# Performance work log

Hardware: AMD Instinct MI355X
Metric: run time of the kernel (lower is better)

Reference implementation:

```python
import jax, jax.numpy as jnp
import numpy as np

EPS = 2e-05
N_H_RDG = 9   # lifting scale grid: h_j = 2**j, j=0..8
N_H_CROP = 3  # group-conv scale support: offsets 0,1,2 (dyadic index shifts)


def _scaled_kernel(w, h):
    """Resample base kernel w [O, I, K] (taps on integers centered at 0) at
    coordinates x/h via linear interpolation -> [O, I, (K-1)*h+1], with the
    R+ Haar-measure normalization 1/h (psi_h(x) = psi(x/h)/h)."""
    K = w.shape[-1]
    Kh = (K - 1) * h + 1
    m = jnp.arange(K, dtype=jnp.float32) - K // 2
    x = (jnp.arange(Kh, dtype=jnp.float32) - Kh // 2) / h
    hat = jnp.maximum(0.0, 1.0 - jnp.abs(x[:, None] - m[None, :]))  # [Kh, K]
    return jnp.einsum('oim,xm->oix', w, hat) / h


def _conv1d_same(x, k):
    pad = (k.shape[-1] - 1) // 2
    return jax.lax.conv_general_dilated(
        x, k, window_strides=(1,), padding=[(pad, pad)],
        dimension_numbers=('NCH', 'OIH', 'NCH'))


def _pool_r1(x, stride):
    # max pool over the spatial (last) axis only: kernel 4, pad 1 each side
    return jax.lax.reduce_window(
        x, -jnp.inf, jax.lax.max,
        window_dimensions=(1, 1, 1, 4), window_strides=(1, 1, 1, stride),
        padding=((0, 0), (0, 0), (0, 0), (1, 1)))


def _bn(x, g, b):
    # BatchNorm2d over [B, C, H_scale, L], training-mode batch stats
    mu = jnp.mean(x, axis=(0, 2, 3), keepdims=True)
    var = jnp.var(x, axis=(0, 2, 3), keepdims=True)
    return (x - mu) * jax.lax.rsqrt(var + EPS) * g[None, :, None, None] + b[None, :, None, None]


def _forward(x, w1, w2, w3, g1, b1, g2, b2, g3, b3, fw1, fb1, fw2, fb2, fw3, fb3):
    B = x.shape[0]
    # --- c1: GConvRdG lifting, scales h_j = 2**j, j=0..8 ---
    out = jnp.stack([_conv1d_same(x, _scaled_kernel(w1, 2 ** j))
                     for j in range(N_H_RDG)], axis=2)      # [B,16,9,16]
    out = _bn(jax.nn.relu(_pool_r1(out, 2)), g1, b1)        # [B,16,9,8]
    # --- c2: GConvGG, h_crop=True: out scale j uses in scales j..j+2 ---
    O2, I2 = w2.shape[0], w2.shape[1]
    w2r = w2.reshape(O2, I2 * N_H_CROP, 3)
    H2 = out.shape[2] - (N_H_CROP - 1)  # 7
    out = jnp.stack([
        _conv1d_same(out[:, :, j:j + N_H_CROP, :].reshape(B, I2 * N_H_CROP, -1),
                     _scaled_kernel(w2r, 2 ** j))
        for j in range(H2)], axis=2)                        # [B,32,7,8]
    out = _bn(jax.nn.relu(_pool_r1(out, 2)), g2, b2)        # [B,32,7,4]
    # --- c3: GConvGG with 1x1 spatial kernel ---
    w3s = w3[:, :, :, 0]  # [64,32,3]
    H3 = out.shape[2] - (N_H_CROP - 1)  # 5
    out = jnp.stack([
        jnp.einsum('oik,bikl->bol', w3s, out[:, :, j:j + N_H_CROP, :]) / (2.0 ** j)
        for j in range(H3)], axis=2)                        # [B,64,5,4]
    out = _bn(jax.nn.relu(_pool_r1(out, 4)), g3, b3)        # [B,64,5,1]
    # --- MLP head (dropout is identity in eval) ---
    out = out.reshape(B, -1)                                # [B,320]
    out = out @ fw1.T + fb1
    out = out @ fw2.T + fb2
    return out @ fw3.T + fb3                                # [B,17]


def setup_inputs() -> dict:
    key = jax.random.key(0)
    ks = jax.random.split(key, 7)
    B = 4096
    x = jax.random.normal(ks[0], (B, 6, 16), dtype=jnp.float32)
    w1 = jax.random.normal(ks[1], (16, 6, 7), dtype=jnp.float32) * (6 * 7) ** -0.5
    w2 = jax.random.normal(ks[2], (32, 16, 3, 3), dtype=jnp.float32) * (16 * 3 * 3) ** -0.5
    w3 = jax.random.normal(ks[3], (64, 32, 3, 1), dtype=jnp.float32) * (32 * 3) ** -0.5
    fw1 = jax.random.normal(ks[4], (16, 320), dtype=jnp.float32) * 320 ** -0.5
    fw2 = jax.random.normal(ks[5], (16, 16), dtype=jnp.float32) * 16 ** -0.5
    fw3 = jax.random.normal(ks[6], (17, 16), dtype=jnp.float32) * 16 ** -0.5
    return {
        'x': x, 'w1': w1, 'w2': w2, 'w3': w3,
        'g1': jnp.ones(16), 'b1': jnp.zeros(16),
        'g2': jnp.ones(32), 'b2': jnp.zeros(32),
        'g3': jnp.ones(64), 'b3': jnp.zeros(64),
        'fw1': fw1, 'fb1': jnp.zeros(16),
        'fw2': fw2, 'fb2': jnp.zeros(16),
        'fw3': fw3, 'fb3': jnp.zeros(17),
    }


def reference(x, w1, w2, w3, g1, b1, g2, b2, g3, b3, fw1, fb1, fw2, fb2, fw3, fb3):
    return _forward(x, w1, w2, w3, g1, b1, g2, b2, g3, b3, fw1, fb1, fw2, fb2, fw3, fb3)
```

## Files before the change

kernel.cpp:

```cpp
#include <hip/hip_runtime.h>

#define EPS 2e-5f

using short8  = __attribute__((ext_vector_type(8))) short;
using floatx4 = __attribute__((ext_vector_type(4))) float;

static __device__ inline unsigned short f2bf(float f) {
    unsigned u = __float_as_uint(f);
    u += 0x7fffu + ((u >> 16) & 1u);
    return (unsigned short)(u >> 16);
}


__global__ void __launch_bounds__(256) k_setup(const float* __restrict__ w1,
                                               unsigned short* __restrict__ W1f,
                                               float* __restrict__ stats) {
    int gid = blockIdx.x * 256 + threadIdx.x;
    if (gid < 256) stats[gid] = 0.f;
    if (gid >= 221184) return;
    int j  = gid / 24576;
    int r  = gid % 24576;
    int T  = r / 1536;
    int r2 = r % 1536;
    int ks = r2 / 512;
    int r3 = r2 % 512;
    int lane = r3 >> 3, e = r3 & 7;
    int n  = T * 16 + (lane & 15);
    int kk = ks * 32 + (lane >> 4) * 8 + e;
    int o = n >> 4, t = n & 15;
    int i = kk >> 4, s = kk & 15;
    int h = 1 << j;
    int d = s - t;
    float val = 0.f;
    if (d >= -3 * h && d <= 3 * h) {
        float df = (float)d / (float)h;
        #pragma unroll
        for (int m = 0; m < 7; ++m) {
            float hat = fmaxf(0.f, 1.f - fabsf(df - (float)(m - 3)));
            val += w1[(o * 6 + i) * 7 + m] * hat;
        }
        val /= (float)h;
    }
    W1f[gid] = f2bf(val);
}

__global__ void __launch_bounds__(256) k1(const float* __restrict__ x,
                                          const unsigned short* __restrict__ W1f,
                                          unsigned short* __restrict__ p1,
                                          float* __restrict__ stats1) {
    int j    = blockIdx.y;
    int wav  = threadIdx.x >> 6;
    int lane = threadIdx.x & 63;
    int msub = wav & 1, nh = wav >> 1;
    int mt   = blockIdx.x * 2 + msub;
    int quad = lane >> 4, l15 = lane & 15;
    floatx4 z = {0.f, 0.f, 0.f, 0.f};
    floatx4 acc[8];
    #pragma unroll
    for (int T = 0; T < 8; ++T) acc[T] = z;
    const float* xr = x + (size_t)(mt * 16 + l15) * 96;
    const short8* Bj = (const short8*)W1f + (size_t)(j * 16) * 3 * 64;
    #pragma unroll
    for (int ks = 0; ks < 3; ++ks) {
        int k0 = ks * 32 + quad * 8;
        floatx4 v0 = *(const floatx4*)(xr + k0);
        floatx4 v1 = *(const floatx4*)(xr + k0 + 4);
        short8 a;
        #pragma unroll
        for (int e = 0; e < 4; ++e) {
            a[e]     = (short)f2bf(v0[e]);
            a[e + 4] = (short)f2bf(v1[e]);
        }
        #pragma unroll
        for (int T = 0; T < 8; ++T) {
            short8 b = Bj[((nh * 8 + T) * 3 + ks) * 64 + lane];
            acc[T] = __builtin_amdgcn_mfma_f32_16x16x32_bf16(a, b, acc[T], 0, 0, 0);
        }
    }
    __shared__ float ls[32];
    if (threadIdx.x < 32) ls[threadIdx.x] = 0.f;
    __syncthreads();
    int mbase = mt * 16 + quad * 4;
    int tp = l15;
    bool act = tp < 8;
    int tpe = tp & 7;
    int base = lane & 48;
    int c0 = base + max(2 * tpe - 1, 0);
    int c1 = base + 2 * tpe;
    int c2 = base + 2 * tpe + 1;
    int c3 = base + min(2 * tpe + 2, 15);
    #pragma unroll
    for (int T = 0; T < 8; ++T) {
        int o = nh * 8 + T;
        float psum = 0.f, pss = 0.f;
        #pragma unroll
        for (int r = 0; r < 4; ++r) {
            float v  = acc[T][r];
            float mx = fmaxf(fmaxf(__shfl(v, c0, 64), __shfl(v, c1, 64)),
                             fmaxf(__shfl(v, c2, 64), __shfl(v, c3, 64)));
            mx = fmaxf(mx, 0.f);
            if (act) {
                p1[(size_t)(mbase + r) * 1152 + o * 72 + j * 8 + tp] = f2bf(mx);
                psum += mx; pss += mx * mx;
            }
        }
        #pragma unroll
        for (int m = 32; m >= 1; m >>= 1) {
            psum += __shfl_xor(psum, m, 64);
            pss  += __shfl_xor(pss,  m, 64);
        }
        if (lane == 0) {
            atomicAdd(&ls[o], psum);
            atomicAdd(&ls[16 + o], pss);
        }
    }
    __syncthreads();
    if (threadIdx.x < 16) {
        atomicAdd(&stats1[threadIdx.x], ls[threadIdx.x]);
        atomicAdd(&stats1[16 + threadIdx.x], ls[16 + threadIdx.x]);
    }
}

__global__ void __launch_bounds__(384) k_bias(const float* __restrict__ w2,
                                              const float* __restrict__ g1,
                                              const float* __restrict__ b1,
                                              const float* __restrict__ stats1,
                                              unsigned short* __restrict__ W2f,
                                              float* __restrict__ bias2,
                                              float invN1) {
    int blk = blockIdx.x;
    int j   = blk >> 8;
    int col = blk & 255;
    int o = col >> 3, t = col & 7;
    int k = threadIdx.x;
    int ic = k >> 3, s = k & 7;
    int i = ic / 3, c = ic % 3;
    float mu  = stats1[i] * invN1;
    float var = stats1[16 + i] * invN1 - mu * mu;
    float rsg = rsqrtf(var + EPS);
    float a1  = g1[i] * rsg;
    float d1  = b1[i] - mu * a1;
    int h = 1 << j;
    int d = s - t;
    float raw = 0.f;
    if (d >= -h && d <= h) {
        float df = (float)d / (float)h;
        #pragma unroll
        for (int m = 0; m < 3; ++m) {
            float hat = fmaxf(0.f, 1.f - fabsf(df - (float)(m - 1)));
            raw += w2[((o * 16 + i) * 3 + c) * 3 + m] * hat;
        }
        raw /= (float)h;
    }
    {
        int T    = col >> 4;
        int lane = (col & 15) + ((k >> 3) & 3) * 16;
        int ks   = k >> 5;
        int e    = k & 7;
        W2f[(((size_t)(j * 16 + T) * 12 + ks) * 64 + lane) * 8 + e] = f2bf(raw * a1);
    }
    __shared__ float red[384];
    red[k] = raw * d1;
    __syncthreads();
    if (k < 128) red[k] += red[k + 128] + red[k + 256];
    __syncthreads();
    for (int st = 64; st >= 1; st >>= 1) {
        if (k < st) red[k] += red[k + st];
        __syncthreads();
    }
    if (k == 0) bias2[j * 256 + col] = red[0];
}

__global__ void __launch_bounds__(256) k2(const unsigned short* __restrict__ p1,
                                          const unsigned short* __restrict__ W2f,
                                          const float* __restrict__ bias2,
                                          unsigned short* __restrict__ p2s,
                                          float* __restrict__ stats2,
                                          int B) {
    int j    = blockIdx.y;
    int wav  = threadIdx.x >> 6;
    int lane = threadIdx.x & 63;
    int nh   = wav & 1, mp = wav >> 1;
    int m0   = blockIdx.x * 64 + mp * 32;
    int quad = lane >> 4, l15 = lane & 15;
    floatx4 z = {0.f, 0.f, 0.f, 0.f};
    floatx4 acc[2][8];
    #pragma unroll
    for (int mi = 0; mi < 2; ++mi)
        #pragma unroll
        for (int T = 0; T < 8; ++T) acc[mi][T] = z;
    const short8* Bj = (const short8*)W2f + (size_t)(j * 16) * 12 * 64;
    const unsigned short* Arow0 = p1 + (size_t)(m0 + l15) * 1152;
    const unsigned short* Arow1 = Arow0 + 16 * 1152;
    #pragma unroll
    for (int ks = 0; ks < 12; ++ks) {
        int k0 = ks * 32 + quad * 8;
        int i  = k0 / 24;
        int c  = (k0 - i * 24) >> 3;
        int off = i * 72 + (j + c) * 8;
        short8 a0 = *(const short8*)(Arow0 + off);
        short8 a1 = *(const short8*)(Arow1 + off);
        #pragma unroll
        for (int T = 0; T < 8; ++T) {
            short8 b = Bj[((nh * 8 + T) * 12 + ks) * 64 + lane];
            acc[0][T] = __builtin_amdgcn_mfma_f32_16x16x32_bf16(a0, b, acc[0][T], 0, 0, 0);
            acc[1][T] = __builtin_amdgcn_mfma_f32_16x16x32_bf16(a1, b, acc[1][T], 0, 0, 0);
        }
    }
    __shared__ float ls[64];
    if (threadIdx.x < 64) ls[threadIdx.x] = 0.f;
    __syncthreads();
    int tp  = lane & 7;
    bool act = tp < 4;
    int tpe = tp & 3;
    int base = lane & 56;
    int c0 = base + max(2 * tpe - 1, 0);
    int c1 = base + 2 * tpe;
    int c2 = base + 2 * tpe + 1;
    int c3 = base + min(2 * tpe + 2, 7);
    #pragma unroll
    for (int T = 0; T < 8; ++T) {
        int n = (nh * 8 + T) * 16 + l15;
        int o = n >> 3;
        float bias = bias2[j * 256 + n];
        float psum = 0.f, pss = 0.f;
        #pragma unroll
        for (int mi = 0; mi < 2; ++mi) {
            int mbase = m0 + mi * 16 + quad * 4;
            #pragma unroll
            for (int r = 0; r < 4; ++r) {
                float v  = acc[mi][T][r] + bias;
                float mx = fmaxf(fmaxf(__shfl(v, c0, 64), __shfl(v, c1, 64)),
                                 fmaxf(__shfl(v, c2, 64), __shfl(v, c3, 64)));
                mx = fmaxf(mx, 0.f);
                if (act) {
                    p2s[(((size_t)j * 4 + tp) * B + mbase + r) * 32 + o] = f2bf(mx);
                    psum += mx; pss += mx * mx;
                }
            }
        }
        #pragma unroll
        for (int m = 0; m < 5; ++m) {
            int msk = (m < 3) ? (1 << m) : (1 << (m + 1));
            psum += __shfl_xor(psum, msk, 64);
            pss  += __shfl_xor(pss,  msk, 64);
        }
        if (lane == 0 || lane == 8) {
            int oo = (nh * 8 + T) * 2 + (lane >> 3);
            atomicAdd(&ls[oo], psum);
            atomicAdd(&ls[32 + oo], pss);
        }
    }
    __syncthreads();
    if (threadIdx.x < 32) {
        atomicAdd(&stats2[threadIdx.x], ls[threadIdx.x]);
        atomicAdd(&stats2[32 + threadIdx.x], ls[32 + threadIdx.x]);
    }
}

__global__ void __launch_bounds__(256) k3(const unsigned short* __restrict__ p2s,
                                          const float* __restrict__ w3,
                                          const float* __restrict__ g2,
                                          const float* __restrict__ b2,
                                          const float* __restrict__ stats2,
                                          float* __restrict__ act3,
                                          float* __restrict__ stats3,
                                          float invN2, int B) {
    int j    = blockIdx.y;
    int wav  = threadIdx.x >> 6;
    int lane = threadIdx.x & 63;
    int msub = wav & 1, nh = wav >> 1;
    int m0   = (blockIdx.x * 2 + msub) * 16;
    int quad = lane >> 4, l15 = lane & 15;
    __shared__ float a2s[32], d2s[32], bias3s[64], ls[128];
    __shared__ unsigned short W3s[6144];
    if (threadIdx.x < 128) ls[threadIdx.x] = 0.f;
    if (threadIdx.x < 32) {
        int i = threadIdx.x;
        float mu  = stats2[i] * invN2;
        float var = stats2[32 + i] * invN2 - mu * mu;
        float rsg = rsqrtf(var + EPS);
        a2s[i] = g2[i] * rsg;
        d2s[i] = b2[i] - mu * a2s[i];
    }
    __syncthreads();
    for (int idx = threadIdx.x; idx < 6144; idx += 256) {
        int e  = idx & 7;
        int ln = (idx >> 3) & 63;
        int fs = idx >> 9;
        int Tg = fs / 3, ks = fs % 3;
        int n = Tg * 16 + (ln & 15);
        int i = (ln >> 4) * 8 + e;
        W3s[idx] = f2bf(w3[n * 96 + i * 3 + ks] * a2s[i]);
    }
    if (threadIdx.x < 64) {
        float s = 0.f;
        for (int i = 0; i < 32; ++i)
            #pragma unroll
            for (int kk = 0; kk < 3; ++kk)
                s = fmaf(w3[threadIdx.x * 96 + i * 3 + kk], d2s[i], s);
        bias3s[threadIdx.x] = s;
    }
    __syncthreads();
    short8 bf[2][3];
    #pragma unroll
    for (int T = 0; T < 2; ++T)
        #pragma unroll
        for (int ks = 0; ks < 3; ++ks)
            bf[T][ks] = *(const short8*)&W3s[(((nh * 2 + T) * 3 + ks) * 64 + lane) * 8];
    floatx4 z = {0.f, 0.f, 0.f, 0.f};
    floatx4 acc[2][3];
    #pragma unroll
    for (int T = 0; T < 2; ++T)
        #pragma unroll
        for (int l = 0; l < 3; ++l) acc[T][l] = z;
    #pragma unroll
    for (int ks = 0; ks < 3; ++ks) {
        int jj = j + ks;
        #pragma unroll
        for (int l = 0; l < 3; ++l) {
            const short8* ap =
                (const short8*)(p2s + ((size_t)(jj * 4 + l) * B + m0 + l15) * 32) + quad;
            short8 a = *ap;
            #pragma unroll
            for (int T = 0; T < 2; ++T)
                acc[T][l] = __builtin_amdgcn_mfma_f32_16x16x32_bf16(a, bf[T][ks],
                                                                    acc[T][l], 0, 0, 0);
        }
    }
    float inv = 1.f / (float)(1 << j);
    int mbase = m0 + quad * 4;
    #pragma unroll
    for (int T = 0; T < 2; ++T) {
        int col = nh * 32 + T * 16 + l15;
        float bias = bias3s[col];
        float psum = 0.f, pss = 0.f;
        #pragma unroll
        for (int r = 0; r < 4; ++r) {
            float v = fmaxf(fmaxf(acc[T][0][r], acc[T][1][r]), acc[T][2][r]);
            v = fmaxf((v + bias) * inv, 0.f);
            act3[(size_t)(mbase + r) * 320 + col * 5 + j] = v;
            psum += v; pss += v * v;
        }
        psum += __shfl_xor(psum, 16, 64); pss += __shfl_xor(pss, 16, 64);
        psum += __shfl_xor(psum, 32, 64); pss += __shfl_xor(pss, 32, 64);
        if (quad == 0) {
            atomicAdd(&ls[col], psum);
            atomicAdd(&ls[64 + col], pss);
        }
    }
    __syncthreads();
    if (threadIdx.x < 64) {
        atomicAdd(&stats3[threadIdx.x], ls[threadIdx.x]);
        atomicAdd(&stats3[64 + threadIdx.x], ls[64 + threadIdx.x]);
    }
}

__global__ void __launch_bounds__(128) k4(const float* __restrict__ act3,
                                          const float* __restrict__ g3,
                                          const float* __restrict__ b3,
                                          const float* __restrict__ stats3,
                                          const float* __restrict__ fw1,
                                          const float* __restrict__ fb1,
                                          const float* __restrict__ fw2,
                                          const float* __restrict__ fb2,
                                          const float* __restrict__ fw3,
                                          const float* __restrict__ fb3,
                                          float* __restrict__ out,
                                          float invN3) {
    __shared__ float a3s[64], d3s[64];
    __shared__ unsigned short W1s[5120];
    __shared__ float fw2s[256], fw3s[272], fb2s[16], fb3s[17], fb1f[16];
    __shared__ float hbuf[2][16][17];
    int tid = threadIdx.x;
    if (tid < 64) {
        float mu  = stats3[tid] * invN3;
        float var = stats3[64 + tid] * invN3 - mu * mu;
        float rsg = rsqrtf(var + EPS);
        a3s[tid] = g3[tid] * rsg;
        d3s[tid] = b3[tid] - mu * a3s[tid];
    }
    __syncthreads();
    for (int idx = tid; idx < 5120; idx += 128) {
        int e  = idx & 7;
        int ln = (idx >> 3) & 63;
        int ks = idx >> 9;
        int n  = ln & 15;
        int k  = ks * 32 + (ln >> 4) * 8 + e;
        W1s[idx] = f2bf(fw1[n * 320 + k] * a3s[k / 5]);
    }
    for (int idx = tid; idx < 256; idx += 128) fw2s[idx] = fw2[idx];
    for (int idx = tid; idx < 272; idx += 128) fw3s[idx] = fw3[idx];
    if (tid < 16) fb2s[tid] = fb2[tid];
    if (tid < 17) fb3s[tid] = fb3[tid];
    if (tid < 16) {
        float s = fb1[tid];
        for (int o = 0; o < 64; ++o) {
            float dd = d3s[o];
            #pragma unroll
            for (int jj = 0; jj < 5; ++jj)
                s = fmaf(fw1[tid * 320 + o * 5 + jj], dd, s);
        }
        fb1f[tid] = s;
    }
    __syncthreads();
    int wav = tid >> 6, lane = tid & 63;
    int quad = lane >> 4, l15 = lane & 15;
    int mt = blockIdx.x * 2 + wav;
    const float* ar = act3 + (size_t)(mt * 16 + l15) * 320;
    floatx4 acc = {0.f, 0.f, 0.f, 0.f};
    #pragma unroll
    for (int ks = 0; ks < 10; ++ks) {
        int k0 = ks * 32 + quad * 8;
        floatx4 v0 = *(const floatx4*)(ar + k0);
        floatx4 v1 = *(const floatx4*)(ar + k0 + 4);
        short8 a;
        #pragma unroll
        for (int e = 0; e < 4; ++e) {
            a[e]     = (short)f2bf(v0[e]);
            a[e + 4] = (short)f2bf(v1[e]);
        }
        short8 b = *(const short8*)&W1s[(ks * 64 + lane) * 8];
        acc = __builtin_amdgcn_mfma_f32_16x16x32_bf16(a, b, acc, 0, 0, 0);
    }
    #pragma unroll
    for (int r = 0; r < 4; ++r)
        hbuf[wav][quad * 4 + r][l15] = acc[r] + fb1f[l15];
    __syncthreads();
    if (lane < 16) {
        int row = l15;
        float hv[16];
        #pragma unroll
        for (int n = 0; n < 16; ++n) hv[n] = hbuf[wav][row][n];
        float h2[16];
        #pragma unroll
        for (int f2 = 0; f2 < 16; ++f2) {
            float s = fb2s[f2];
            #pragma unroll
            for (int n = 0; n < 16; ++n) s = fmaf(fw2s[f2 * 16 + n], hv[n], s);
            h2[f2] = s;
        }
        float* orow = out + (size_t)(mt * 16 + row) * 17;
        #pragma unroll
        for (int f3 = 0; f3 < 17; ++f3) {
            float s = fb3s[f3];
            #pragma unroll
            for (int n = 0; n < 16; ++n) s = fmaf(fw3s[f3 * 16 + n], h2[n], s);
            orow[f3] = s;
        }
    }
}

extern "C" void kernel_launch(void* const* d_in, const int* in_sizes, int n_in,
                              void* d_out, int out_size, void* d_ws, size_t ws_size,
                              hipStream_t stream) {
    (void)n_in; (void)out_size; (void)ws_size;
    const float* x   = (const float*)d_in[0];
    const float* w1  = (const float*)d_in[1];
    const float* w2  = (const float*)d_in[2];
    const float* w3  = (const float*)d_in[3];
    const float* g1  = (const float*)d_in[4];
    const float* b1  = (const float*)d_in[5];
    const float* g2  = (const float*)d_in[6];
    const float* b2  = (const float*)d_in[7];
    const float* g3  = (const float*)d_in[8];
    const float* b3  = (const float*)d_in[9];
    const float* fw1 = (const float*)d_in[10];
    const float* fb1 = (const float*)d_in[11];
    const float* fw2 = (const float*)d_in[12];
    const float* fb2 = (const float*)d_in[13];
    const float* fw3 = (const float*)d_in[14];
    const float* fb3 = (const float*)d_in[15];
    float* out = (float*)d_out;

    int B = in_sizes[0] / 96;

    char* wsb = (char*)d_ws;
    float*          stats  = (float*)wsb;
    unsigned short* W1f    = (unsigned short*)(wsb + 1024);
    unsigned short* W2f    = W1f + 221184;
    float*          bias2  = (float*)(W2f + 688128);
    unsigned short* p1     = (unsigned short*)(bias2 + 1792);
    unsigned short* p2s    = p1 + (size_t)B * 1152;
    float*          act3   = (float*)(p2s + (size_t)B * 896);

    float* stats1 = stats;
    float* stats2 = stats + 32;
    float* stats3 = stats + 96;

    float invN1 = 1.f / (float)(B * 72);
    float invN2 = 1.f / (float)(B * 28);
    float invN3 = 1.f / (float)(B * 5);

    k_setup<<<864, 256, 0, stream>>>(w1, W1f, stats);
    k1<<<dim3(B / 32, 9), 256, 0, stream>>>(x, W1f, p1, stats1);
    k_bias<<<7 * 256, 384, 0, stream>>>(w2, g1, b1, stats1, W2f, bias2, invN1);
    k2<<<dim3(B / 64, 7), 256, 0, stream>>>(p1, W2f, bias2, p2s, stats2, B);
    k3<<<dim3(B / 32, 5), 256, 0, stream>>>(p2s, w3, g2, b2, stats2, act3, stats3,
                                            invN2, B);
    k4<<<B / 32, 128, 0, stream>>>(act3, g3, b3, stats3, fw1, fb1, fw2, fb2, fw3, fb3,
                                   out, invN3);
}
```

Baseline: 204.1 us.

## Fuse all stages into one cooperative persistent kernel with grid syncs

Replaces the six separate kernel launches with a single cooperative persistent kernel that runs every stage in turn and separates them with grid-wide syncs. It also changes the intermediate layouts to scale-major bf16 tiles, written coalesced through shared memory, and stores act3 as bf16 instead of fp32. The aim is to remove launch gaps and shrink intermediate memory traffic. In exchange it pays for grid barriers and limits parallelism to the number of resident blocks, capped at 512.

```diff
diff --git a/kernel.cpp b/kernel.cpp
--- a/kernel.cpp
+++ b/kernel.cpp
@@ -1,6 +1,9 @@
 #include <hip/hip_runtime.h>
+#include <hip/hip_cooperative_groups.h>
 
 #define EPS 2e-5f
+
+namespace cg = cooperative_groups;
 
 using short8  = __attribute__((ext_vector_type(8))) short;
 using floatx4 = __attribute__((ext_vector_type(4))) float;
@@ -12,441 +15,485 @@
 }
 
 
-__global__ void __launch_bounds__(256) k_setup(const float* __restrict__ w1,
-                                               unsigned short* __restrict__ W1f,
-                                               float* __restrict__ stats) {
-    int gid = blockIdx.x * 256 + threadIdx.x;
-    if (gid < 256) stats[gid] = 0.f;
-    if (gid >= 221184) return;
-    int j  = gid / 24576;
-    int r  = gid % 24576;
-    int T  = r / 1536;
-    int r2 = r % 1536;
-    int ks = r2 / 512;
-    int r3 = r2 % 512;
-    int lane = r3 >> 3, e = r3 & 7;
-    int n  = T * 16 + (lane & 15);
-    int kk = ks * 32 + (lane >> 4) * 8 + e;
-    int o = n >> 4, t = n & 15;
-    int i = kk >> 4, s = kk & 15;
-    int h = 1 << j;
-    int d = s - t;
-    float val = 0.f;
-    if (d >= -3 * h && d <= 3 * h) {
-        float df = (float)d / (float)h;
+struct P2S { float ls[32]; unsigned short ptile[32][16][8]; };
+struct P3S { float a1[16]; float d1[16]; };
+struct P4S { float ls[64]; unsigned short ptile[4][64][32]; };
+struct P5S { float a2s[32], d2s[32], bias3s[64], ls[128];
+             unsigned short W3s[6144]; unsigned short atile[32][64]; };
+struct P6S { float a3s[64], d3s[64];
+             float fw2s[256], fw3s[272], fb2s[16], fb3s[17], fb1f[16];
+             float hbuf[4][16][17]; unsigned short W1s[5120]; };
+union SmemU { P2S p2; P3S p3; P4S p4; P5S p5; P6S p6; };
+
+__global__ void __launch_bounds__(256, 2)
+mega(const float* __restrict__ x,   const float* __restrict__ w1,
+     const float* __restrict__ w2,  const float* __restrict__ w3,
+     const float* __restrict__ g1,  const float* __restrict__ b1,
+     const float* __restrict__ g2,  const float* __restrict__ b2,
+     const float* __restrict__ g3,  const float* __restrict__ b3,
+     const float* __restrict__ fw1, const float* __restrict__ fb1,
+     const float* __restrict__ fw2, const float* __restrict__ fb2,
+     const float* __restrict__ fw3, const float* __restrict__ fb3,
+     float* __restrict__ out,
+     float* __restrict__ stats, unsigned short* __restrict__ W1f,
+     unsigned short* __restrict__ W2f, float* __restrict__ bias2,
+     unsigned short* __restrict__ p1, unsigned short* __restrict__ p2s,
+     unsigned short* __restrict__ act3, int B) {
+    cg::grid_group gg = cg::this_grid();
+    __shared__ SmemU sm;
+    const int tid  = threadIdx.x;
+    const int bid  = blockIdx.x;
+    const int nblk = gridDim.x;
+    const int wav  = tid >> 6;
+    const int lane = tid & 63;
+    const int quad = lane >> 4, l15 = lane & 15;
+    float* stats1 = stats;
+    float* stats2 = stats + 32;
+    float* stats3 = stats + 96;
+    const float invN1 = 1.f / (float)(B * 72);
+    const float invN2 = 1.f / (float)(B * 28);
+    const float invN3 = 1.f / (float)(B * 5);
+
+    {
+        int g0 = bid * 256 + tid;
+        if (g0 < 256) stats[g0] = 0.f;
+        for (int gid = g0; gid < 221184; gid += nblk * 256) {
+            int j  = gid / 24576;
+            int r  = gid % 24576;
+            int T  = r / 1536;
+            int r2 = r % 1536;
+            int ks = r2 / 512;
+            int r3 = r2 % 512;
+            int ln = r3 >> 3, e = r3 & 7;
+            int n  = T * 16 + (ln & 15);
+            int kk = ks * 32 + (ln >> 4) * 8 + e;
+            int o = n >> 4, t = n & 15;
+            int i = kk >> 4, s = kk & 15;
+            int h = 1 << j;
+            int d = s - t;
+            float val = 0.f;
+            if (d >= -3 * h && d <= 3 * h) {
+                float df = (float)d / (float)h;
+                #pragma unroll
+                for (int m = 0; m < 7; ++m) {
+                    float hat = fmaxf(0.f, 1.f - fabsf(df - (float)(m - 3)));
+                    val += w1[(o * 6 + i) * 7 + m] * hat;
+                }
+                val /= (float)h;
+            }
+            W1f[gid] = f2bf(val);
+        }
+    }
+    gg.sync();
+
+    {
+        int t32max = B / 32;
+        int msub = wav & 1, nh = wav >> 1;
+        for (int wi = bid; wi < 9 * t32max; wi += nblk) {
+            int j = wi / t32max, t32 = wi - j * t32max;
+            __syncthreads();
+            if (tid < 32) sm.p2.ls[tid] = 0.f;
+            int mt = t32 * 2 + msub;
+            floatx4 z = {0.f, 0.f, 0.f, 0.f};
+            floatx4 acc[8];
+            #pragma unroll
+            for (int T = 0; T < 8; ++T) acc[T] = z;
+            const float* xr = x + (size_t)(mt * 16 + l15) * 96;
+            const short8* Bj = (const short8*)W1f + (size_t)(j * 16) * 3 * 64;
+            #pragma unroll
+            for (int ks = 0; ks < 3; ++ks) {
+                int k0 = ks * 32 + quad * 8;
+                floatx4 v0 = *(const floatx4*)(xr + k0);
+                floatx4 v1 = *(const floatx4*)(xr + k0 + 4);
+                short8 a;
+                #pragma unroll
+                for (int e = 0; e < 4; ++e) {
+                    a[e]     = (short)f2bf(v0[e]);
+                    a[e + 4] = (short)f2bf(v1[e]);
+                }
+                #pragma unroll
+                for (int T = 0; T < 8; ++T) {
+                    short8 b = Bj[((nh * 8 + T) * 3 + ks) * 64 + lane];
+                    acc[T] = __builtin_amdgcn_mfma_f32_16x16x32_bf16(a, b, acc[T], 0, 0, 0);
+                }
+            }
+            __syncthreads();
+            int tp = l15;
+            bool act = tp < 8;
+            int tpe = tp & 7;
+            int base = lane & 48;
+            int c0 = base + max(2 * tpe - 1, 0);
+            int c1 = base + 2 * tpe;
+            int c2 = base + 2 * tpe + 1;
+            int c3 = base + min(2 * tpe + 2, 15);
+            int row_l = msub * 16 + quad * 4;
+            #pragma unroll
+            for (int T = 0; T < 8; ++T) {
+                int o = nh * 8 + T;
+                float psum = 0.f, pss = 0.f;
+                #pragma unroll
+                for (int r = 0; r < 4; ++r) {
+                    float v  = acc[T][r];
+                    float mx = fmaxf(fmaxf(__shfl(v, c0, 64), __shfl(v, c1, 64)),
+                                     fmaxf(__shfl(v, c2, 64), __shfl(v, c3, 64)));
+                    mx = fmaxf(mx, 0.f);
+                    if (act) {
+                        sm.p2.ptile[row_l + r][o][tp] = f2bf(mx);
+                        psum += mx; pss += mx * mx;
+                    }
+                }
+                #pragma unroll
+                for (int m = 32; m >= 1; m >>= 1) {
+                    psum += __shfl_xor(psum, m, 64);
+                    pss  += __shfl_xor(pss,  m, 64);
+                }
+                if (lane == 0) {
+                    atomicAdd(&sm.p2.ls[o], psum);
+                    atomicAdd(&sm.p2.ls[16 + o], pss);
+                }
+            }
+            __syncthreads();
+            unsigned short* dst = p1 + ((size_t)j * B + t32 * 32) * 128;
+            #pragma unroll
+            for (int u = 0; u < 2; ++u) {
+                int c = tid + u * 256;
+                int rr = c >> 4, oo = c & 15;
+                *(short8*)(dst + (size_t)rr * 128 + oo * 8) =
+                    *(const short8*)&sm.p2.ptile[rr][oo][0];
+            }
+            if (tid < 16) {
+                atomicAdd(&stats1[tid], sm.p2.ls[tid]);
+                atomicAdd(&stats1[16 + tid], sm.p2.ls[16 + tid]);
+            }
+        }
+    }
+    gg.sync();
+
+    {
+        if (tid < 16) {
+            float mu  = stats1[tid] * invN1;
+            float var = stats1[16 + tid] * invN1 - mu * mu;
+            float rsg = rsqrtf(var + EPS);
+            float a1  = g1[tid] * rsg;
+            sm.p3.a1[tid] = a1;
+            sm.p3.d1[tid] = b1[tid] - mu * a1;
+        }
+        __syncthreads();
+        for (int gid = bid * 256 + tid; gid < 688128; gid += nblk * 256) {
+            int j  = gid / 98304;
+            int r  = gid % 98304;
+            int T  = r / 6144;
+            int r2 = r % 6144;
+            int ks = r2 / 512;
+            int r3 = r2 % 512;
+            int ln = r3 >> 3, e = r3 & 7;
+            int col = T * 16 + (ln & 15);
+            int k   = ks * 32 + ((ln >> 4) << 3) + e;
+            int o = col >> 3, t = col & 7;
+            int ic = k >> 3, s = k & 7;
+            int i = ic / 3, c = ic % 3;
+            int h = 1 << j;
+            int d = s - t;
+            float raw = 0.f;
+            if (d >= -h && d <= h) {
+                float df = (float)d / (float)h;
+                #pragma unroll
+                for (int m = 0; m < 3; ++m) {
+                    float hat = fmaxf(0.f, 1.f - fabsf(df - (float)(m - 1)));
+                    raw += w2[((o * 16 + i) * 3 + c) * 3 + m] * hat;
+                }
+                raw /= (float)h;
+            }
+            W2f[gid] = f2bf(raw * sm.p3.a1[i]);
+        }
+        for (int e = bid * 4 + wav; e < 1792; e += nblk * 4) {
+            int j = e >> 8, col = e & 255;
+            int o = col >> 3, t = col & 7;
+            int h = 1 << j;
+            float s = 0.f;
+            #pragma unroll
+            for (int u = 0; u < 6; ++u) {
+                int k = lane + 64 * u;
+                int ic = k >> 3, ss = k & 7;
+                int i = ic / 3, c = ic % 3;
+                int d = ss - t;
+                float raw = 0.f;
+                if (d >= -h && d <= h) {
+                    float df = (float)d / (float)h;
+                    #pragma unroll
+                    for (int m = 0; m < 3; ++m) {
+                        float hat = fmaxf(0.f, 1.f - fabsf(df - (float)(m - 1)));
+                        raw += w2[((o * 16 + i) * 3 + c) * 3 + m] * hat;
+                    }
+                    raw /= (float)h;
+                }
+                s = fmaf(raw, sm.p3.d1[i], s);
+            }
+            #pragma unroll
+            for (int m = 32; m >= 1; m >>= 1) s += __shfl_xor(s, m, 64);
+            if (lane == 0) bias2[e] = s;
+        }
+    }
+    gg.sync();
+
+    {
+        int t64max = B / 64;
+        int nh = wav & 1, mp = wav >> 1;
+        for (int wi = bid; wi < 7 * t64max; wi += nblk) {
+            int j = wi / t64max, t64 = wi - j * t64max;
+            __syncthreads();
+            if (tid < 64) sm.p4.ls[tid] = 0.f;
+            int m0 = t64 * 64 + mp * 32;
+            floatx4 z = {0.f, 0.f, 0.f, 0.f};
+            floatx4 acc[2][8];
+            #pragma unroll
+            for (int mi = 0; mi < 2; ++mi)
+                #pragma unroll
+                for (int T = 0; T < 8; ++T) acc[mi][T] = z;
+            const short8* Bj = (const short8*)W2f + (size_t)(j * 16) * 12 * 64;
+            #pragma unroll
+            for (int ks = 0; ks < 12; ++ks) {
+                int k0 = ks * 32 + quad * 8;
+                int i  = k0 / 24;
+                int c  = (k0 - i * 24) >> 3;
+                const unsigned short* ab =
+                    p1 + ((size_t)(j + c) * B + m0 + l15) * 128 + i * 8;
+                short8 a0 = *(const short8*)ab;
+                short8 a1 = *(const short8*)(ab + 16 * 128);
+                #pragma unroll
+                for (int T = 0; T < 8; ++T) {
+                    short8 b = Bj[((nh * 8 + T) * 12 + ks) * 64 + lane];
+                    acc[0][T] = __builtin_amdgcn_mfma_f32_16x16x32_bf16(a0, b, acc[0][T], 0, 0, 0);
+                    acc[1][T] = __builtin_amdgcn_mfma_f32_16x16x32_bf16(a1, b, acc[1][T], 0, 0, 0);
+                }
+            }
+            __syncthreads();
+            int tp  = lane & 7;
+            bool act = tp < 4;
+            int tpe = tp & 3;
+            int base = lane & 56;
+            int c0 = base + max(2 * tpe - 1, 0);
+            int c1 = base + 2 * tpe;
+            int c2 = base + 2 * tpe + 1;
+            int c3 = base + min(2 * tpe + 2, 7);
+            #pragma unroll
+            for (int T = 0; T < 8; ++T) {
+                int n = (nh * 8 + T) * 16 + l15;
+                int o = n >> 3;
+                float bias = bias2[j * 256 + n];
+                float psum = 0.f, pss = 0.f;
+                #pragma unroll
+                for (int mi = 0; mi < 2; ++mi) {
+                    int rbase = mp * 32 + mi * 16 + quad * 4;
+                    #pragma unroll
+                    for (int r = 0; r < 4; ++r) {
+                        float v  = acc[mi][T][r] + bias;
+                        float mx = fmaxf(fmaxf(__shfl(v, c0, 64), __shfl(v, c1, 64)),
+                                         fmaxf(__shfl(v, c2, 64), __shfl(v, c3, 64)));
+                        mx = fmaxf(mx, 0.f);
+                        if (act) {
+                            sm.p4.ptile[tp][rbase + r][o] = f2bf(mx);
+                            psum += mx; pss += mx * mx;
+                        }
+                    }
+                }
+                #pragma unroll
+                for (int m = 0; m < 5; ++m) {
+                    int msk = (m < 3) ? (1 << m) : (1 << (m + 1));
+                    psum += __shfl_xor(psum, msk, 64);
+                    pss  += __shfl_xor(pss,  msk, 64);
+                }
+                if (lane == 0 || lane == 8) {
+                    int oo = (nh * 8 + T) * 2 + (lane >> 3);
+                    atomicAdd(&sm.p4.ls[oo], psum);
+                    atomicAdd(&sm.p4.ls[32 + oo], pss);
+                }
+            }
+            __syncthreads();
+            #pragma unroll
+            for (int u = 0; u < 4; ++u) {
+                int c = tid + u * 256;
+                int tpp = c >> 8, rem = c & 255;
+                int rr = rem >> 2, oq = rem & 3;
+                *(short8*)(p2s + ((size_t)(j * 4 + tpp) * B + t64 * 64 + rr) * 32 + oq * 8) =
+                    *(const short8*)&sm.p4.ptile[tpp][rr][oq * 8];
+            }
+            if (tid < 32) {
+                atomicAdd(&stats2[tid], sm.p4.ls[tid]);
+                atomicAdd(&stats2[32 + tid], sm.p4.ls[32 + tid]);
+            }
+        }
+    }
+    gg.sync();
+
+    {
+        if (tid < 32) {
+            float mu  = stats2[tid] * invN2;
+            float var = stats2[32 + tid] * invN2 - mu * mu;
+            float rsg = rsqrtf(var + EPS);
+            sm.p5.a2s[tid] = g2[tid] * rsg;
+            sm.p5.d2s[tid] = b2[tid] - mu * sm.p5.a2s[tid];
+        }
+        __syncthreads();
+        for (int idx = tid; idx < 6144; idx += 256) {
+            int e  = idx & 7;
+            int ln = (idx >> 3) & 63;
+            int fs = idx >> 9;
+            int Tg = fs / 3, ks = fs % 3;
+            int n = Tg * 16 + (ln & 15);
+            int i = (ln >> 4) * 8 + e;
+            sm.p5.W3s[idx] = f2bf(w3[n * 96 + i * 3 + ks] * sm.p5.a2s[i]);
+        }
+        if (tid < 64) {
+            float s = 0.f;
+            for (int i = 0; i < 32; ++i)
+                #pragma unroll
+                for (int kk = 0; kk < 3; ++kk)
+                    s = fmaf(w3[tid * 96 + i * 3 + kk], sm.p5.d2s[i], s);
+            sm.p5.bias3s[tid] = s;
+        }
+        __syncthreads();
+        int msub = wav & 1, nh = wav >> 1;
+        short8 bf[2][3];
         #pragma unroll
-        for (int m = 0; m < 7; ++m) {
-            float hat = fmaxf(0.f, 1.f - fabsf(df - (float)(m - 3)));
-            val += w1[(o * 6 + i) * 7 + m] * hat;
-        }
-        val /= (float)h;
+        for (int T = 0; T < 2; ++T)
+            #pragma unroll
+            for (int ks = 0; ks < 3; ++ks)
+                bf[T][ks] = *(const short8*)&sm.p5.W3s[(((nh * 2 + T) * 3 + ks) * 64 + lane) * 8];
+        int t32max = B / 32;
+        for (int wi = bid; wi < 5 * t32max; wi += nblk) {
+            int j = wi / t32max, t32 = wi - j * t32max;
+            __syncthreads();
+            if (tid < 128) sm.p5.ls[tid] = 0.f;
+            int m0 = (t32 * 2 + msub) * 16;
+            floatx4 z = {0.f, 0.f, 0.f, 0.f};
+            floatx4 acc[2][3];
+            #pragma unroll
+            for (int T = 0; T < 2; ++T)
+                #pragma unroll
+                for (int l = 0; l < 3; ++l) acc[T][l] = z;
+            #pragma unroll
+            for (int ks = 0; ks < 3; ++ks) {
+                int jj = j + ks;
+                #pragma unroll
+                for (int l = 0; l < 3; ++l) {
+                    short8 a = *(const short8*)(p2s +
+                        ((size_t)(jj * 4 + l) * B + m0 + l15) * 32 + quad * 8);
+                    #pragma unroll
+                    for (int T = 0; T < 2; ++T)
+                        acc[T][l] = __builtin_amdgcn_mfma_f32_16x16x32_bf16(a, bf[T][ks],
+                                                                            acc[T][l], 0, 0, 0);
+                }
+            }
+            __syncthreads();
+            float inv = 1.f / (float)(1 << j);
+            int row_l = msub * 16 + quad * 4;
+            #pragma unroll
+            for (int T = 0; T < 2; ++T) {
+                int col = nh * 32 + T * 16 + l15;
+                float bias = sm.p5.bias3s[col];
+                float psum = 0.f, pss = 0.f;
+                #pragma unroll
+                for (int r = 0; r < 4; ++r) {
+                    float v = fmaxf(fmaxf(acc[T][0][r], acc[T][1][r]), acc[T][2][r]);
+                    v = fmaxf((v + bias) * inv, 0.f);
+                    sm.p5.atile[row_l + r][col] = f2bf(v);
+                    psum += v; pss += v * v;
+                }
+                psum += __shfl_xor(psum, 16, 64); pss += __shfl_xor(pss, 16, 64);
+                psum += __shfl_xor(psum, 32, 64); pss += __shfl_xor(pss, 32, 64);
+                if (quad == 0) {
+                    atomicAdd(&sm.p5.ls[col], psum);
+                    atomicAdd(&sm.p5.ls[64 + col], pss);
+                }
+            }
+            __syncthreads();
+            {
+                int rr = tid >> 3, oq = tid & 7;
+                *(short8*)(act3 + ((size_t)j * B + t32 * 32 + rr) * 64 + oq * 8) =
+                    *(const short8*)&sm.p5.atile[rr][oq * 8];
+            }
+            if (tid < 64) {
+                atomicAdd(&stats3[tid], sm.p5.ls[tid]);
+                atomicAdd(&stats3[64 + tid], sm.p5.ls[64 + tid]);
+            }
+        }
     }
-    W1f[gid] = f2bf(val);
-}
-
-__global__ void __launch_bounds__(256) k1(const float* __restrict__ x,
-                                          const unsigned short* __restrict__ W1f,
-                                          unsigned short* __restrict__ p1,
-                                          float* __restrict__ stats1) {
-    int j    = blockIdx.y;
-    int wav  = threadIdx.x >> 6;
-    int lane = threadIdx.x & 63;
-    int msub = wav & 1, nh = wav >> 1;
-    int mt   = blockIdx.x * 2 + msub;
-    int quad = lane >> 4, l15 = lane & 15;
-    floatx4 z = {0.f, 0.f, 0.f, 0.f};
-    floatx4 acc[8];
-    #pragma unroll
-    for (int T = 0; T < 8; ++T) acc[T] = z;
-    const float* xr = x + (size_t)(mt * 16 + l15) * 96;
-    const short8* Bj = (const short8*)W1f + (size_t)(j * 16) * 3 * 64;
-    #pragma unroll
-    for (int ks = 0; ks < 3; ++ks) {
-        int k0 = ks * 32 + quad * 8;
-        floatx4 v0 = *(const floatx4*)(xr + k0);
-        floatx4 v1 = *(const floatx4*)(xr + k0 + 4);
-        short8 a;
-        #pragma unroll
-        for (int e = 0; e < 4; ++e) {
-            a[e]     = (short)f2bf(v0[e]);
-            a[e + 4] = (short)f2bf(v1[e]);
-        }
-        #pragma unroll
-        for (int T = 0; T < 8; ++T) {
-            short8 b = Bj[((nh * 8 + T) * 3 + ks) * 64 + lane];
-            acc[T] = __builtin_amdgcn_mfma_f32_16x16x32_bf16(a, b, acc[T], 0, 0, 0);
-        }
-    }
-    __shared__ float ls[32];
-    if (threadIdx.x < 32) ls[threadIdx.x] = 0.f;
-    __syncthreads();
-    int mbase = mt * 16 + quad * 4;
-    int tp = l15;
-    bool act = tp < 8;
-    int tpe = tp & 7;
-    int base = lane & 48;
-    int c0 = base + max(2 * tpe - 1, 0);
-    int c1 = base + 2 * tpe;
-    int c2 = base + 2 * tpe + 1;
-    int c3 = base + min(2 * tpe + 2, 15);
-    #pragma unroll
-    for (int T = 0; T < 8; ++T) {
-        int o = nh * 8 + T;
-        float psum = 0.f, pss = 0.f;
-        #pragma unroll
-        for (int r = 0; r < 4; ++r) {
-            float v  = acc[T][r];
-            float mx = fmaxf(fmaxf(__shfl(v, c0, 64), __shfl(v, c1, 64)),
-                             fmaxf(__shfl(v, c2, 64), __shfl(v, c3, 64)));
-            mx = fmaxf(mx, 0.f);
-            if (act) {
-                p1[(size_t)(mbase + r) * 1152 + o * 72 + j * 8 + tp] = f2bf(mx);
-                psum += mx; pss += mx * mx;
-            }
-        }
-        #pragma unroll
-        for (int m = 32; m >= 1; m >>= 1) {
-            psum += __shfl_xor(psum, m, 64);
-            pss  += __shfl_xor(pss,  m, 64);
-        }
-        if (lane == 0) {
-            atomicAdd(&ls[o], psum);
-            atomicAdd(&ls[16 + o], pss);
-        }
-    }
-    __syncthreads();
-    if (threadIdx.x < 16) {
-        atomicAdd(&stats1[threadIdx.x], ls[threadIdx.x]);
-        atomicAdd(&stats1[16 + threadIdx.x], ls[16 + threadIdx.x]);
-    }
-}
-
-__global__ void __launch_bounds__(384) k_bias(const float* __restrict__ w2,
-                                              const float* __restrict__ g1,
-                                              const float* __restrict__ b1,
-                                              const float* __restrict__ stats1,
-                                              unsigned short* __restrict__ W2f,
-                                              float* __restrict__ bias2,
-                                              float invN1) {
-    int blk = blockIdx.x;
-    int j   = blk >> 8;
-    int col = blk & 255;
-    int o = col >> 3, t = col & 7;
-    int k = threadIdx.x;
-    int ic = k >> 3, s = k & 7;
-    int i = ic / 3, c = ic % 3;
-    float mu  = stats1[i] * invN1;
-    float var = stats1[16 + i] * invN1 - mu * mu;
-    float rsg = rsqrtf(var + EPS);
-    float a1  = g1[i] * rsg;
-    float d1  = b1[i] - mu * a1;
-    int h = 1 << j;
-    int d = s - t;
-    float raw = 0.f;
-    if (d >= -h && d <= h) {
-        float df = (float)d / (float)h;
-        #pragma unroll
-        for (int m = 0; m < 3; ++m) {
-            float hat = fmaxf(0.f, 1.f - fabsf(df - (float)(m - 1)));
-            raw += w2[((o * 16 + i) * 3 + c) * 3 + m] * hat;
-        }
-        raw /= (float)h;
-    }
+    gg.sync();
+
     {
-        int T    = col >> 4;
-        int lane = (col & 15) + ((k >> 3) & 3) * 16;
-        int ks   = k >> 5;
-        int e    = k & 7;
-        W2f[(((size_t)(j * 16 + T) * 12 + ks) * 64 + lane) * 8 + e] = f2bf(raw * a1);
-    }
-    __shared__ float red[384];
-    red[k] = raw * d1;
-    __syncthreads();
-    if (k < 128) red[k] += red[k + 128] + red[k + 256];
-    __syncthreads();
-    for (int st = 64; st >= 1; st >>= 1) {
-        if (k < st) red[k] += red[k + st];
+        if (tid < 64) {
+            float mu  = stats3[tid] * invN3;
+            float var = stats3[64 + tid] * invN3 - mu * mu;
+            float rsg = rsqrtf(var + EPS);
+            sm.p6.a3s[tid] = g3[tid] * rsg;
+            sm.p6.d3s[tid] = b3[tid] - mu * sm.p6.a3s[tid];
+        }
         __syncthreads();
-    }
-    if (k == 0) bias2[j * 256 + col] = red[0];
-}
-
-__global__ void __launch_bounds__(256) k2(const unsigned short* __restrict__ p1,
-                                          const unsigned short* __restrict__ W2f,
-                                          const float* __restrict__ bias2,
-                                          unsigned short* __restrict__ p2s,
-                                          float* __restrict__ stats2,
-                                          int B) {
-    int j    = blockIdx.y;
-    int wav  = threadIdx.x >> 6;
-    int lane = threadIdx.x & 63;
-    int nh   = wav & 1, mp = wav >> 1;
-    int m0   = blockIdx.x * 64 + mp * 32;
-    int quad = lane >> 4, l15 = lane & 15;
-    floatx4 z = {0.f, 0.f, 0.f, 0.f};
-    floatx4 acc[2][8];
-    #pragma unroll
-    for (int mi = 0; mi < 2; ++mi)
-        #pragma unroll
-        for (int T = 0; T < 8; ++T) acc[mi][T] = z;
-    const short8* Bj = (const short8*)W2f + (size_t)(j * 16) * 12 * 64;
-    const unsigned short* Arow0 = p1 + (size_t)(m0 + l15) * 1152;
-    const unsigned short* Arow1 = Arow0 + 16 * 1152;
-    #pragma unroll
-    for (int ks = 0; ks < 12; ++ks) {
-        int k0 = ks * 32 + quad * 8;
-        int i  = k0 / 24;
-        int c  = (k0 - i * 24) >> 3;
-        int off = i * 72 + (j + c) * 8;
-        short8 a0 = *(const short8*)(Arow0 + off);
-        short8 a1 = *(const short8*)(Arow1 + off);
-        #pragma unroll
-        for (int T = 0; T < 8; ++T) {
-            short8 b = Bj[((nh * 8 + T) * 12 + ks) * 64 + lane];
-            acc[0][T] = __builtin_amdgcn_mfma_f32_16x16x32_bf16(a0, b, acc[0][T], 0, 0, 0);
-            acc[1][T] = __builtin_amdgcn_mfma_f32_16x16x32_bf16(a1, b, acc[1][T], 0, 0, 0);
-        }
-    }
-    __shared__ float ls[64];
-    if (threadIdx.x < 64) ls[threadIdx.x] = 0.f;
-    __syncthreads();
-    int tp  = lane & 7;
-    bool act = tp < 4;
-    int tpe = tp & 3;
-    int base = lane & 56;
-    int c0 = base + max(2 * tpe - 1, 0);
-    int c1 = base + 2 * tpe;
-    int c2 = base + 2 * tpe + 1;
-    int c3 = base + min(2 * tpe + 2, 7);
-    #pragma unroll
-    for (int T = 0; T < 8; ++T) {
-        int n = (nh * 8 + T) * 16 + l15;
-        int o = n >> 3;
-        float bias = bias2[j * 256 + n];
-        float psum = 0.f, pss = 0.f;
-        #pragma unroll
-        for (int mi = 0; mi < 2; ++mi) {
-            int mbase = m0 + mi * 16 + quad * 4;
-            #pragma unroll
-            for (int r = 0; r < 4; ++r) {
-                float v  = acc[mi][T][r] + bias;
-                float mx = fmaxf(fmaxf(__shfl(v, c0, 64), __shfl(v, c1, 64)),
-                                 fmaxf(__shfl(v, c2, 64), __shfl(v, c3, 64)));
-                mx = fmaxf(mx, 0.f);
-                if (act) {
-                    p2s[(((size_t)j * 4 + tp) * B + mbase + r) * 32 + o] = f2bf(mx);
-                    psum += mx; pss += mx * mx;
-                }
-            }
-        }
-        #pragma unroll
-        for (int m = 0; m < 5; ++m) {
-            int msk = (m < 3) ? (1 << m) : (1 << (m + 1));
-            psum += __shfl_xor(psum, msk, 64);
-            pss  += __shfl_xor(pss,  msk, 64);
-        }
-        if (lane == 0 || lane == 8) {
-            int oo = (nh * 8 + T) * 2 + (lane >> 3);
-            atomicAdd(&ls[oo], psum);
-            atomicAdd(&ls[32 + oo], pss);
-        }
-    }
-    __syncthreads();
-    if (threadIdx.x < 32) {
-        atomicAdd(&stats2[threadIdx.x], ls[threadIdx.x]);
-        atomicAdd(&stats2[32 + threadIdx.x], ls[32 + threadIdx.x]);
-    }
-}
-
-__global__ void __launch_bounds__(256) k3(const unsigned short* __restrict__ p2s,
-                                          const float* __restrict__ w3,
-                                          const float* __restrict__ g2,
-                                          const float* __restrict__ b2,
-                                          const float* __restrict__ stats2,
-                                          float* __restrict__ act3,
-                                          float* __restrict__ stats3,
-                                          float invN2, int B) {
-    int j    = blockIdx.y;
-    int wav  = threadIdx.x >> 6;
-    int lane = threadIdx.x & 63;
-    int msub = wav & 1, nh = wav >> 1;
-    int m0   = (blockIdx.x * 2 + msub) * 16;
-    int quad = lane >> 4, l15 = lane & 15;
-    __shared__ float a2s[32], d2s[32], bias3s[64], ls[128];
-    __shared__ unsigned short W3s[6144];
-    if (threadIdx.x < 128) ls[threadIdx.x] = 0.f;
-    if (threadIdx.x < 32) {
-        int i = threadIdx.x;
-        float mu  = stats2[i] * invN2;
-        float var = stats2[32 + i] * invN2 - mu * mu;
-        float rsg = rsqrtf(var + EPS);
-        a2s[i] = g2[i] * rsg;
-        d2s[i] = b2[i] - mu * a2s[i];
-    }
-    __syncthreads();
-    for (int idx = threadIdx.x; idx < 6144; idx += 256) {
-        int e  = idx & 7;
-        int ln = (idx >> 3) & 63;
-        int fs = idx >> 9;
-        int Tg = fs / 3, ks = fs % 3;
-        int n = Tg * 16 + (ln & 15);
-        int i = (ln >> 4) * 8 + e;
-        W3s[idx] = f2bf(w3[n * 96 + i * 3 + ks] * a2s[i]);
-    }
-    if (threadIdx.x < 64) {
-        float s = 0.f;
-        for (int i = 0; i < 32; ++i)
-            #pragma unroll
-            for (int kk = 0; kk < 3; ++kk)
-                s = fmaf(w3[threadIdx.x * 96 + i * 3 + kk], d2s[i], s);
-        bias3s[threadIdx.x] = s;
-    }
-    __syncthreads();
-    short8 bf[2][3];
-    #pragma unroll
-    for (int T = 0; T < 2; ++T)
-        #pragma unroll
-        for (int ks = 0; ks < 3; ++ks)
-            bf[T][ks] = *(const short8*)&W3s[(((nh * 2 + T) * 3 + ks) * 64 + lane) * 8];
-    floatx4 z = {0.f, 0.f, 0.f, 0.f};
-    floatx4 acc[2][3];
-    #pragma unroll
-    for (int T = 0; T < 2; ++T)
-        #pragma unroll
-        for (int l = 0; l < 3; ++l) acc[T][l] = z;
-    #pragma unroll
-    for (int ks = 0; ks < 3; ++ks) {
-        int jj = j + ks;
-        #pragma unroll
-        for (int l = 0; l < 3; ++l) {
-            const short8* ap =
-                (const short8*)(p2s + ((size_t)(jj * 4 + l) * B + m0 + l15) * 32) + quad;
-            short8 a = *ap;
-            #pragma unroll
-            for (int T = 0; T < 2; ++T)
-                acc[T][l] = __builtin_amdgcn_mfma_f32_16x16x32_bf16(a, bf[T][ks],
-                                                                    acc[T][l], 0, 0, 0);
-        }
-    }
-    float inv = 1.f / (float)(1 << j);
-    int mbase = m0 + quad * 4;
-    #pragma unroll
-    for (int T = 0; T < 2; ++T) {
-        int col = nh * 32 + T * 16 + l15;
-        float bias = bias3s[col];
-        float psum = 0.f, pss = 0.f;
-        #pragma unroll
-        for (int r = 0; r < 4; ++r) {
-            float v = fmaxf(fmaxf(acc[T][0][r], acc[T][1][r]), acc[T][2][r]);
-            v = fmaxf((v + bias) * inv, 0.f);
-            act3[(size_t)(mbase + r) * 320 + col * 5 + j] = v;
-            psum += v; pss += v * v;
-        }
-        psum += __shfl_xor(psum, 16, 64); pss += __shfl_xor(pss, 16, 64);
-        psum += __shfl_xor(psum, 32, 64); pss += __shfl_xor(pss, 32, 64);
-        if (quad == 0) {
-            atomicAdd(&ls[col], psum);
-            atomicAdd(&ls[64 + col], pss);
-        }
-    }
-    __syncthreads();
-    if (threadIdx.x < 64) {
-        atomicAdd(&stats3[threadIdx.x], ls[threadIdx.x]);
-        atomicAdd(&stats3[64 + threadIdx.x], ls[64 + threadIdx.x]);
-    }
-}
-
-__global__ void __launch_bounds__(128) k4(const float* __restrict__ act3,
-                                          const float* __restrict__ g3,
-                                          const float* __restrict__ b3,
-                                          const float* __restrict__ stats3,
-                                          const float* __restrict__ fw1,
-                                          const float* __restrict__ fb1,
-                                          const float* __restrict__ fw2,
-                                          const float* __restrict__ fb2,
-                                          const float* __restrict__ fw3,
-                                          const float* __restrict__ fb3,
-                                          float* __restrict__ out,
-                                          float invN3) {
-    __shared__ float a3s[64], d3s[64];
-    __shared__ unsigned short W1s[5120];
-    __shared__ float fw2s[256], fw3s[272], fb2s[16], fb3s[17], fb1f[16];
-    __shared__ float hbuf[2][16][17];
-    int tid = threadIdx.x;
-    if (tid < 64) {
-        float mu  = stats3[tid] * invN3;
-        float var = stats3[64 + tid] * invN3 - mu * mu;
-        float rsg = rsqrtf(var + EPS);
-        a3s[tid] = g3[tid] * rsg;
-        d3s[tid] = b3[tid] - mu * a3s[tid];
-    }
-    __syncthreads();
-    for (int idx = tid; idx < 5120; idx += 128) {
-        int e  = idx & 7;
-        int ln = (idx >> 3) & 63;
-        int ks = idx >> 9;
-        int n  = ln & 15;
-        int k  = ks * 32 + (ln >> 4) * 8 + e;
-        W1s[idx] = f2bf(fw1[n * 320 + k] * a3s[k / 5]);
-    }
-    for (int idx = tid; idx < 256; idx += 128) fw2s[idx] = fw2[idx];
-    for (int idx = tid; idx < 272; idx += 128) fw3s[idx] = fw3[idx];
-    if (tid < 16) fb2s[tid] = fb2[tid];
-    if (tid < 17) fb3s[tid] = fb3[tid];
-    if (tid < 16) {
-        float s = fb1[tid];
-        for (int o = 0; o < 64; ++o) {
-            float dd = d3s[o];
-            #pragma unroll
-            for (int jj = 0; jj < 5; ++jj)
-                s = fmaf(fw1[tid * 320 + o * 5 + jj], dd, s);
-        }
-        fb1f[tid] = s;
-    }
-    __syncthreads();
-    int wav = tid >> 6, lane = tid & 63;
-    int quad = lane >> 4, l15 = lane & 15;
-    int mt = blockIdx.x * 2 + wav;
-    const float* ar = act3 + (size_t)(mt * 16 + l15) * 320;
-    floatx4 acc = {0.f, 0.f, 0.f, 0.f};
-    #pragma unroll
-    for (int ks = 0; ks < 10; ++ks) {
-        int k0 = ks * 32 + quad * 8;
-        floatx4 v0 = *(const floatx4*)(ar + k0);
-        floatx4 v1 = *(const floatx4*)(ar + k0 + 4);
-        short8 a;
-        #pragma unroll
-        for (int e = 0; e < 4; ++e) {
-            a[e]     = (short)f2bf(v0[e]);
-            a[e + 4] = (short)f2bf(v1[e]);
-        }
-        short8 b = *(const short8*)&W1s[(ks * 64 + lane) * 8];
-        acc = __builtin_amdgcn_mfma_f32_16x16x32_bf16(a, b, acc, 0, 0, 0);
-    }
-    #pragma unroll
-    for (int r = 0; r < 4; ++r)
-        hbuf[wav][quad * 4 + r][l15] = acc[r] + fb1f[l15];
-    __syncthreads();
-    if (lane < 16) {
-        int row = l15;
-        float hv[16];
-        #pragma unroll
-        for (int n = 0; n < 16; ++n) hv[n] = hbuf[wav][row][n];
-        float h2[16];
-        #pragma unroll
-        for (int f2 = 0; f2 < 16; ++f2) {
-            float s = fb2s[f2];
-            #pragma unroll
-            for (int n = 0; n < 16; ++n) s = fmaf(fw2s[f2 * 16 + n], hv[n], s);
-            h2[f2] = s;
-        }
-        float* orow = out + (size_t)(mt * 16 + row) * 17;
-        #pragma unroll
-        for (int f3 = 0; f3 < 17; ++f3) {
-            float s = fb3s[f3];
-            #pragma unroll
-            for (int n = 0; n < 16; ++n) s = fmaf(fw3s[f3 * 16 + n], h2[n], s);
-            orow[f3] = s;
+        for (int idx = tid; idx < 5120; idx += 256) {
+            int e  = idx & 7;
+            int ln = (idx >> 3) & 63;
+            int fs = idx >> 9;
+            int j = fs >> 1, ks = fs & 1;
+            int n = ln & 15;
+            int o = ks * 32 + (ln >> 4) * 8 + e;
+            sm.p6.W1s[idx] = f2bf(fw1[n * 320 + o * 5 + j] * sm.p6.a3s[o]);
+        }
+        if (tid < 256) sm.p6.fw2s[tid] = fw2[tid];
+        for (int idx = tid; idx < 272; idx += 256) sm.p6.fw3s[idx] = fw3[idx];
+        if (tid < 16) sm.p6.fb2s[tid] = fb2[tid];
+        if (tid < 17) sm.p6.fb3s[tid] = fb3[tid];
+        if (tid >= 32 && tid < 48) {
+            int f = tid - 32;
+            float s = fb1[f];
+            for (int o = 0; o < 64; ++o) {
+                float dd = sm.p6.d3s[o];
+                #pragma unroll
+                for (int jj = 0; jj < 5; ++jj)
+                    s = fmaf(fw1[f * 320 + o * 5 + jj], dd, s);
+            }
+            sm.p6.fb1f[f] = s;
+        }
+        __syncthreads();
+        for (int tq = bid; tq < B / 64; tq += nblk) {
+            int mt = tq * 4 + wav;
+            floatx4 acc = {0.f, 0.f, 0.f, 0.f};
+            #pragma unroll
+            for (int j = 0; j < 5; ++j)
+                #pragma unroll
+                for (int ks = 0; ks < 2; ++ks) {
+                    short8 a = *(const short8*)(act3 +
+                        ((size_t)j * B + mt * 16 + l15) * 64 + ks * 32 + quad * 8);
+                    short8 b = *(const short8*)&sm.p6.W1s[((j * 2 + ks) * 64 + lane) * 8];
+                    acc = __builtin_amdgcn_mfma_f32_16x16x32_bf16(a, b, acc, 0, 0, 0);
+                }
+            #pragma unroll
+            for (int r = 0; r < 4; ++r)
+                sm.p6.hbuf[wav][quad * 4 + r][l15] = acc[r] + sm.p6.fb1f[l15];
+            __syncthreads();
+            if (lane < 16) {
+                int row = l15;
+                float hv[16];
+                #pragma unroll
+                for (int n = 0; n < 16; ++n) hv[n] = sm.p6.hbuf[wav][row][n];
+                float h2[16];
+                #pragma unroll
+                for (int f2 = 0; f2 < 16; ++f2) {
+                    float s = sm.p6.fb2s[f2];
+                    #pragma unroll
+                    for (int n = 0; n < 16; ++n) s = fmaf(sm.p6.fw2s[f2 * 16 + n], hv[n], s);
+                    h2[f2] = s;
+                }
+                float* orow = out + (size_t)(mt * 16 + row) * 17;
+                #pragma unroll
+                for (int f3 = 0; f3 < 17; ++f3) {
+                    float s = sm.p6.fb3s[f3];
+                    #pragma unroll
+                    for (int n = 0; n < 16; ++n) s = fmaf(sm.p6.fw3s[f3 * 16 + n], h2[n], s);
+                    orow[f3] = s;
+                }
+            }
+            __syncthreads();
         }
     }
 }
@@ -476,28 +523,30 @@
     int B = in_sizes[0] / 96;
 
     char* wsb = (char*)d_ws;
-    float*          stats  = (float*)wsb;
-    unsigned short* W1f    = (unsigned short*)(wsb + 1024);
-    unsigned short* W2f    = W1f + 221184;
-    float*          bias2  = (float*)(W2f + 688128);
-    unsigned short* p1     = (unsigned short*)(bias2 + 1792);
-    unsigned short* p2s    = p1 + (size_t)B * 1152;
-    float*          act3   = (float*)(p2s + (size_t)B * 896);
-
-    float* stats1 = stats;
-    float* stats2 = stats + 32;
-    float* stats3 = stats + 96;
-
-    float invN1 = 1.f / (float)(B * 72);
-    float invN2 = 1.f / (float)(B * 28);
-    float invN3 = 1.f / (float)(B * 5);
-
-    k_setup<<<864, 256, 0, stream>>>(w1, W1f, stats);
-    k1<<<dim3(B / 32, 9), 256, 0, stream>>>(x, W1f, p1, stats1);
-    k_bias<<<7 * 256, 384, 0, stream>>>(w2, g1, b1, stats1, W2f, bias2, invN1);
-    k2<<<dim3(B / 64, 7), 256, 0, stream>>>(p1, W2f, bias2, p2s, stats2, B);
-    k3<<<dim3(B / 32, 5), 256, 0, stream>>>(p2s, w3, g2, b2, stats2, act3, stats3,
-                                            invN2, B);
-    k4<<<B / 32, 128, 0, stream>>>(act3, g3, b3, stats3, fw1, fb1, fw2, fb2, fw3, fb3,
-                                   out, invN3);
+    float*          stats = (float*)wsb;
+    unsigned short* W1f   = (unsigned short*)(wsb + 1024);
+    unsigned short* W2f   = W1f + 221184;
+    float*          bias2 = (float*)(W2f + 688128);
+    unsigned short* p1    = (unsigned short*)(bias2 + 1792);
+    unsigned short* p2s   = p1 + (size_t)9 * B * 128;
+    unsigned short* act3  = p2s + (size_t)28 * B * 32;
+
+    int maxPerCU = 0;
+    hipOccupancyMaxActiveBlocksPerMultiprocessor(&maxPerCU, (const void*)mega, 256, 0);
+    if (maxPerCU < 1) maxPerCU = 1;
+    int numCU = 0;
+    hipDeviceGetAttribute(&numCU, hipDeviceAttributeMultiprocessorCount, 0);
+    if (numCU <= 0) numCU = 256;
+    int NB = maxPerCU * numCU;
+    if (NB > 512) NB = 512;
+
+    void* kargs[] = {
+        (void*)&x, (void*)&w1, (void*)&w2, (void*)&w3,
+        (void*)&g1, (void*)&b1, (void*)&g2, (void*)&b2,
+        (void*)&g3, (void*)&b3, (void*)&fw1, (void*)&fb1,
+        (void*)&fw2, (void*)&fb2, (void*)&fw3, (void*)&fb3,
+        (void*)&out, (void*)&stats, (void*)&W1f, (void*)&W2f,
+        (void*)&bias2, (void*)&p1, (void*)&p2s, (void*)&act3, (void*)&B
+    };
+    hipLaunchCooperativeKernel((void*)mega, dim3(NB), dim3(256), kargs, 0, stream);
 }
```

Result: slower. 399.4 us (+95.7%).
